# Kernel optimization log

Measured on AMD Instinct MI355X. Metric: run time of the kernel, lower is better.

## Reference

```python
import jax, jax.numpy as jnp
import numpy as np

TOP_K = 4

def setup_inputs() -> dict:
    key = jax.random.key(0)
    ks = jax.random.split(key, 10)
    s = 0.02
    return {
        "x": jax.random.normal(ks[0], (4, 1024, 2048), jnp.float32),
        "expert_bias": jnp.zeros((64,), jnp.float32),
        "router_w": jax.random.normal(ks[1], (64, 2048), jnp.float32) * s,
        "gate_w": jax.random.normal(ks[2], (8192, 2048), jnp.float32) * s,
        "up_w": jax.random.normal(ks[3], (8192, 2048), jnp.float32) * s,
        "down_w": jax.random.normal(ks[4], (2048, 8192), jnp.float32) * s,
        "w_down": jax.random.normal(ks[5], (512, 2048), jnp.float32) * s,
        "w_up": jax.random.normal(ks[6], (2048, 512), jnp.float32) * s,
        "experts_w12": jax.random.normal(ks[7], (64, 512, 2048), jnp.float32) * s,
        "experts_w3": jax.random.normal(ks[8], (64, 1024, 512), jnp.float32) * s,
    }


def reference(x, expert_bias, router_w, gate_w, up_w, down_w, w_down, w_up, experts_w12, experts_w3):
    B, S, D = x.shape
    E = router_w.shape[0]
    K = TOP_K
    h = x.reshape(-1, D)            # [N, D]
    N = h.shape[0]
    NK = N * K

    # --- router (fp32) ---
    logits = h @ router_w.T          # [N, E]
    scores = jax.nn.sigmoid(logits)
    z_loss = jnp.mean(logits * logits) * 1e-4
    sel = scores + expert_bias
    _, topk_idx = jax.lax.top_k(sel, K)                      # [N, K]
    topk_logits = jnp.take_along_axis(logits, topk_idx, axis=1)
    gating = jax.nn.softmax(topk_logits, axis=-1)            # [N, K]

    # --- shared SwiGLU expert ---
    shared = (jax.nn.silu(h @ gate_w.T) * (h @ up_w.T)) @ down_w.T   # [N, D]

    # --- bottleneck down projection ---
    hd = h @ w_down.T                # [N, bottle]
    Bn = hd.shape[1]

    # --- dispatch: sort tokens by expert, capacity max_load per expert ---
    flat = topk_idx.reshape(-1)                      # [NK]
    perm = jnp.argsort(flat)                         # stable sort
    sorted_e = flat[perm]
    counts = jnp.bincount(flat, length=E)
    ptr = jnp.cumsum(counts) - counts                # start offset per expert
    local = jnp.arange(NK) - ptr[sorted_e]           # rank within expert
    max_load = (NK // E // 8 + 6) * 8                # static python int
    num_slots = E * max_load
    mask = local < max_load
    slots = sorted_e * max_load + local
    tok = jnp.repeat(jnp.arange(N), K)               # token id per routed slot

    # reverse_map[slot] = token index (N = dummy)
    rm = jnp.full((num_slots + 1,), N, dtype=jnp.int32)
    rm = rm.at[jnp.where(mask, slots, num_slots)].set(tok[perm].astype(jnp.int32))
    reverse_map = rm[:num_slots]

    hwd = jnp.concatenate([hd, jnp.zeros((1, Bn), hd.dtype)], axis=0)
    padding = hwd[reverse_map].reshape(E, max_load, Bn)

    # --- grouped expert GEMMs ---
    h12 = jnp.einsum('emb,ebf->emf', padding, experts_w12)   # [E, L, 2*F]
    h1, h2 = jnp.split(h12, 2, axis=-1)
    pout = jnp.einsum('emf,efb->emb', jax.nn.silu(h1) * h2, experts_w3)
    pout = pout.reshape(-1, Bn)                              # [num_slots, bottle]

    # --- combine: gather back per (token, k) slot and mix with gating ---
    powd = jnp.concatenate([pout, jnp.zeros((1, Bn), pout.dtype)], axis=0)
    gm = jnp.full((NK + 1,), num_slots, dtype=jnp.int32)
    gm = gm.at[jnp.where(mask, perm, NK)].set(jnp.where(mask, slots, num_slots).astype(jnp.int32))
    gather_map = gm[:NK]
    gathered = powd[gather_map].reshape(N, K, Bn)
    routed_b = jnp.einsum('nk,nkb->nb', gating, gathered)
    routed = routed_b @ w_up.T                               # [N, D]

    # eval mode: route_scale = 1.0, moe_scale = 0.5 (one shared expert), aux_loss = 0
    out = (shared + routed) * 0.5
    return out.reshape(B, S, D), z_loss
```

## Files before the change

### kernel.cpp

```cpp
#include <hip/hip_runtime.h>
#include <math.h>

#define NTOK 4096
#define DMODEL 2048
#define ENUM 64
#define HSH 8192
#define BND 512
#define FEXP 1024
#define MAXL 304
#define EPAD 384
#define ECH 16

typedef float f32x4 __attribute__((ext_vector_type(4)));
using bf16x8 = __attribute__((ext_vector_type(8))) __bf16;

typedef const __attribute__((address_space(1))) unsigned int cgu32;
typedef __attribute__((address_space(3))) unsigned int lu32;
#define GLOAD16(g, l) __builtin_amdgcn_global_load_lds((cgu32*)(g), (lu32*)(l), 16, 0, 0)

__device__ __forceinline__ unsigned short f2bf(float f) {
    union { float f; unsigned int u; } v; v.f = f;
    unsigned int u = v.u;
    return (unsigned short)((u + 0x7FFFu + ((u >> 16) & 1u)) >> 16);
}
__device__ __forceinline__ float bf2f(unsigned short s) {
    union { unsigned int u; float f; } v; v.u = ((unsigned int)s) << 16;
    return v.f;
}

__global__ __launch_bounds__(256) void init_kernel(float* zacc, int* slot2tok, unsigned short* hdz) {
    int i = blockIdx.x * 256 + threadIdx.x;
    if (i == 0) *zacc = 0.f;
    if (i < ENUM * MAXL) slot2tok[i] = NTOK;
    if (i < BND) hdz[i] = 0;
}

__global__ __launch_bounds__(256) void convert_kernel(
    const float* __restrict__ in, unsigned short* __restrict__ out, long long n)
{
    long long stride = (long long)gridDim.x * 256 * 8;
    for (long long i = ((long long)blockIdx.x * 256 + threadIdx.x) * 8; i < n; i += stride) {
        float4 a = *(const float4*)(in + i);
        float4 b = *(const float4*)(in + i + 4);
        union { unsigned short s[8]; uint4 v; } o;
        o.s[0] = f2bf(a.x); o.s[1] = f2bf(a.y); o.s[2] = f2bf(a.z); o.s[3] = f2bf(a.w);
        o.s[4] = f2bf(b.x); o.s[5] = f2bf(b.y); o.s[6] = f2bf(b.z); o.s[7] = f2bf(b.w);
        *(uint4*)(out + i) = o.v;
    }
}

__global__ __launch_bounds__(256) void tconv_kernel(
    const float* __restrict__ in, unsigned short* __restrict__ out, int Kd, int Nd)
{
    __shared__ float t[32][33];
    size_t zoff = (size_t)blockIdx.z * Kd * Nd;
    in += zoff; out += zoff;
    int n0 = blockIdx.x * 32, k0 = blockIdx.y * 32;
    int r = threadIdx.x >> 3, c = (threadIdx.x & 7) * 4;
    float4 v = *(const float4*)(in + (size_t)(k0 + r) * Nd + n0 + c);
    t[r][c] = v.x; t[r][c + 1] = v.y; t[r][c + 2] = v.z; t[r][c + 3] = v.w;
    __syncthreads();
    ushort4 o;
    o.x = f2bf(t[c + 0][r]); o.y = f2bf(t[c + 1][r]);
    o.z = f2bf(t[c + 2][r]); o.w = f2bf(t[c + 3][r]);
    *(ushort4*)(out + (size_t)(n0 + r) * Kd + k0 + c) = o;
}

__global__ __launch_bounds__(256) void router_kernel(
    const float* __restrict__ x, const float* __restrict__ rw,
    const float* __restrict__ bias, int* __restrict__ topk_idx,
    float* __restrict__ gating, float* __restrict__ zacc)
{
    int n = blockIdx.x;
    __shared__ float hrow[DMODEL];
    __shared__ float partial[ENUM][4];
    const float* hx = x + (size_t)n * DMODEL;
    for (int i = threadIdx.x; i < DMODEL; i += 256) hrow[i] = hx[i];
    __syncthreads();
    int e = threadIdx.x & 63;
    int p = threadIdx.x >> 6;
    const float4* wr4 = (const float4*)(rw + (size_t)e * DMODEL + p * 512);
    const float4* h4 = (const float4*)(hrow + p * 512);
    float s = 0.f;
    for (int i = 0; i < 128; i++) {
        float4 a = h4[i]; float4 b = wr4[i];
        s += a.x * b.x + a.y * b.y + a.z * b.z + a.w * b.w;
    }
    partial[e][p] = s;
    __syncthreads();
    if (threadIdx.x < 64) {
        float logit = partial[e][0] + partial[e][1] + partial[e][2] + partial[e][3];
        float sel = 1.f / (1.f + expf(-logit)) + bias[e];
        float zsq = logit * logit;
        for (int off = 32; off; off >>= 1) zsq += __shfl_down(zsq, off);
        if (e == 0) atomicAdd(zacc, zsq);
        float cur = sel;
        float ch_logit[4]; int ch_idx[4];
        for (int kk = 0; kk < 4; kk++) {
            float v = cur; int idx = e;
            for (int off = 1; off < 64; off <<= 1) {
                float v2 = __shfl_xor(v, off);
                int i2 = __shfl_xor(idx, off);
                if (v2 > v || (v2 == v && i2 < idx)) { v = v2; idx = i2; }
            }
            ch_idx[kk] = idx;
            ch_logit[kk] = __shfl(logit, idx);
            if (e == idx) cur = -1e30f;
        }
        if (e == 0) {
            float mx = ch_logit[0];
            for (int kk = 1; kk < 4; kk++) mx = fmaxf(mx, ch_logit[kk]);
            float se = 0.f, ex[4];
            for (int kk = 0; kk < 4; kk++) { ex[kk] = expf(ch_logit[kk] - mx); se += ex[kk]; }
            for (int kk = 0; kk < 4; kk++) {
                topk_idx[n * 4 + kk] = ch_idx[kk];
                gating[n * 4 + kk] = ex[kk] / se;
            }
        }
    }
}

__global__ __launch_bounds__(256) void rank_kernel(
    const int* __restrict__ topk_idx, int* __restrict__ slot2tok, int* __restrict__ gmap)
{
    int e = blockIdx.x;
    __shared__ int wsum[4];
    int tid = threadIdx.x;
    int lane = tid & 63, w = tid >> 6;
    int running = 0;
    for (int c = 0; c < NTOK * 4; c += 256) {
        int i = c + tid;
        int fl = topk_idx[i];
        bool m = (fl == e);
        unsigned long long bal = __ballot(m);
        int prefix = __popcll(bal & ((1ULL << lane) - 1ULL));
        if (lane == 0) wsum[w] = __popcll(bal);
        __syncthreads();
        int wbase = 0;
        for (int j = 0; j < w; j++) wbase += wsum[j];
        int total = wsum[0] + wsum[1] + wsum[2] + wsum[3];
        if (m) {
            int rank = running + wbase + prefix;
            int tok = i >> 2;
            if (rank < MAXL) {
                slot2tok[e * MAXL + rank] = tok;
                gmap[i] = e * MAXL + rank;
            } else gmap[i] = -1;
        }
        running += total;
        __syncthreads();
    }
}

template<int GATHER, int EPI>
__global__ __launch_bounds__(256) void gemm2(
    const unsigned short* __restrict__ A, long long aZ, int lda,
    const int* __restrict__ gtab,
    const unsigned short* __restrict__ Bm, long long bZ, int ldb,
    void* __restrict__ Cb, long long cZ, int ldc,
    int M, int K)
{
    __shared__ unsigned short As[2][128 * 64];
    __shared__ unsigned short Bs[2][128 * 64];
    const int z = blockIdx.z;
    const int m0 = blockIdx.y * 128;
    const int n0 = blockIdx.x * 128;
    const int tid = threadIdx.x;
    const int lane = tid & 63;
    const int w = tid >> 6;
    const int wm = (w >> 1) * 64;
    const int wn = (w & 1) * 64;

    const unsigned short* Ab = A + (GATHER ? (size_t)0 : (size_t)z * aZ);
    const unsigned short* Bb = Bm + (size_t)z * bZ;

    size_t asrc[4], bsrc[4];
    int ldso[4];
#pragma unroll
    for (int i = 0; i < 4; i++) {
        int u = i * 256 + tid;
        int r = u >> 3;
        int ce = ((u & 7) ^ (r & 7)) * 8;
        ldso[i] = u * 8;
        if constexpr (GATHER) {
            int mr = m0 + r;
            int tok = (mr < M) ? gtab[(size_t)z * MAXL + mr] : NTOK;
            asrc[i] = (size_t)tok * lda + ce;
        } else {
            asrc[i] = (size_t)(m0 + r) * lda + ce;
        }
        bsrc[i] = (size_t)(n0 + r) * ldb + ce;
    }

    const int lrow = lane & 15;
    const int kg = lane >> 4;
    const int mk = (lrow & 7) << 4;
    int arx[4], brx[4];
#pragma unroll
    for (int t = 0; t < 4; t++) {
        arx[t] = (wm + t * 16 + lrow) * 128;
        brx[t] = (wn + t * 16 + lrow) * 128;
    }

    f32x4 acc[4][4];
#pragma unroll
    for (int a = 0; a < 4; a++)
#pragma unroll
        for (int b = 0; b < 4; b++) acc[a][b] = (f32x4)0.f;

#pragma unroll
    for (int i = 0; i < 4; i++) GLOAD16(Ab + asrc[i], &As[0][ldso[i]]);
#pragma unroll
    for (int i = 0; i < 4; i++) GLOAD16(Bb + bsrc[i], &Bs[0][ldso[i]]);
    __syncthreads();

    int cur = 0;
    for (int k0 = 0; k0 < K; k0 += 64) {
        const int kn = k0 + 64;
        if (kn < K) {
            const int nxt = cur ^ 1;
#pragma unroll
            for (int i = 0; i < 4; i++) GLOAD16(Ab + asrc[i] + kn, &As[nxt][ldso[i]]);
#pragma unroll
            for (int i = 0; i < 4; i++) GLOAD16(Bb + bsrc[i] + kn, &Bs[nxt][ldso[i]]);
        }
        const char* Abase = (const char*)&As[cur][0];
        const char* Bbase = (const char*)&Bs[cur][0];
#pragma unroll
        for (int ks = 0; ks < 2; ks++) {
            const int cb = (ks * 64 + kg * 16) ^ mk;
            bf16x8 a[4], b[4];
#pragma unroll
            for (int t = 0; t < 4; t++) {
                a[t] = *(const bf16x8*)(Abase + arx[t] + cb);
                b[t] = *(const bf16x8*)(Bbase + brx[t] + cb);
            }
#pragma unroll
            for (int ni = 0; ni < 4; ni++)
#pragma unroll
                for (int mi = 0; mi < 4; mi++)
                    acc[mi][ni] = __builtin_amdgcn_mfma_f32_16x16x32_bf16(a[mi], b[ni], acc[mi][ni], 0, 0, 0);
        }
        __syncthreads();
        cur ^= 1;
    }

    const int rb0 = m0 + wm + (kg << 2);
#pragma unroll
    for (int mi = 0; mi < 4; mi++)
#pragma unroll
        for (int ni = 0; ni < 4; ni++) {
            int col = n0 + wn + ni * 16 + lrow;
#pragma unroll
            for (int r = 0; r < 4; r++) {
                int row = rb0 + mi * 16 + r;
                if (row < M) {
                    size_t ci = (size_t)z * cZ + (size_t)row * ldc + col;
                    float v = acc[mi][ni][r];
                    if constexpr (EPI == 0) {
                        ((unsigned short*)Cb)[ci] = f2bf(v);
                    } else if constexpr (EPI == 1) {
                        unsigned short* cp = (unsigned short*)Cb + ci;
                        float g = bf2f(*cp);
                        *cp = f2bf(g / (1.f + expf(-g)) * v);
                    } else if constexpr (EPI == 2) {
                        ((float*)Cb)[ci] = v;
                    } else {
                        float* cp = (float*)Cb + ci;
                        *cp = (*cp + v) * 0.5f;
                    }
                }
            }
        }
}

__global__ __launch_bounds__(256) void siluact_kernel(
    const unsigned short* __restrict__ h12, unsigned short* __restrict__ act)
{
    int e = blockIdx.y, m = blockIdx.x;
    const unsigned short* hr = h12 + ((size_t)e * EPAD + m) * 2048;
    unsigned short* ar = act + ((size_t)e * EPAD + m) * 1024;
    int j = threadIdx.x * 4;
    ushort4 h1 = *(const ushort4*)(hr + j);
    ushort4 h2 = *(const ushort4*)(hr + 1024 + j);
    ushort4 o;
    float v;
    v = bf2f(h1.x); o.x = f2bf(v / (1.f + expf(-v)) * bf2f(h2.x));
    v = bf2f(h1.y); o.y = f2bf(v / (1.f + expf(-v)) * bf2f(h2.y));
    v = bf2f(h1.z); o.z = f2bf(v / (1.f + expf(-v)) * bf2f(h2.z));
    v = bf2f(h1.w); o.w = f2bf(v / (1.f + expf(-v)) * bf2f(h2.w));
    *(ushort4*)(ar + j) = o;
}

__global__ __launch_bounds__(256) void gather_kernel(
    const unsigned short* __restrict__ pout, const int* __restrict__ gmap,
    const float* __restrict__ gating, unsigned short* __restrict__ routed_b)
{
    int n = blockIdx.x;
    int j = threadIdx.x * 2;
    float a0 = 0.f, a1 = 0.f;
#pragma unroll
    for (int kk = 0; kk < 4; kk++) {
        int slot = gmap[n * 4 + kk];
        float g = gating[n * 4 + kk];
        if (slot >= 0) {
            const unsigned short* pr = pout + (size_t)slot * BND + j;
            a0 += g * bf2f(pr[0]);
            a1 += g * bf2f(pr[1]);
        }
    }
    routed_b[(size_t)n * BND + j] = f2bf(a0);
    routed_b[(size_t)n * BND + j + 1] = f2bf(a1);
}

__global__ void zloss_kernel(const float* zacc, float* out) {
    out[0] = zacc[0] * (1.0e-4f / (float)(NTOK * ENUM));
}

extern "C" void kernel_launch(void* const* d_in, const int* in_sizes, int n_in,
                              void* d_out, int out_size, void* d_ws, size_t ws_size,
                              hipStream_t stream)
{
    const float* x      = (const float*)d_in[0];
    const float* ebias  = (const float*)d_in[1];
    const float* rw     = (const float*)d_in[2];
    const float* gate_w = (const float*)d_in[3];
    const float* up_w   = (const float*)d_in[4];
    const float* down_w = (const float*)d_in[5];
    const float* w_down = (const float*)d_in[6];
    const float* w_up   = (const float*)d_in[7];
    const float* w12    = (const float*)d_in[8];
    const float* w3     = (const float*)d_in[9];
    float* out = (float*)d_out;

    char* ws = (char*)d_ws;
    size_t off = 0;
    auto alloc = [&](size_t b) { size_t o = off; off += (b + 255) & ~(size_t)255; return o; };
    float* zacc     = (float*)(ws + alloc(4));
    int*   topk     = (int*)(ws + alloc((size_t)NTOK * 4 * 4));
    float* gating   = (float*)(ws + alloc((size_t)NTOK * 4 * 4));
    int*   gmap     = (int*)(ws + alloc((size_t)NTOK * 4 * 4));
    int*   slot2tok = (int*)(ws + alloc((size_t)ENUM * MAXL * 4));
    unsigned short* xb     = (unsigned short*)(ws + alloc((size_t)NTOK * DMODEL * 2));
    unsigned short* hd     = (unsigned short*)(ws + alloc((size_t)(NTOK + 1) * BND * 2));
    unsigned short* rb     = (unsigned short*)(ws + alloc((size_t)NTOK * BND * 2));
    unsigned short* wdownb = (unsigned short*)(ws + alloc((size_t)BND * DMODEL * 2));
    unsigned short* wupb   = (unsigned short*)(ws + alloc((size_t)DMODEL * BND * 2));
    unsigned short* wbuf   = (unsigned short*)(ws + alloc((size_t)HSH * DMODEL * 2));
    unsigned short* H1     = (unsigned short*)(ws + alloc((size_t)NTOK * HSH * 2));
    unsigned short* h12  = H1;
    unsigned short* act  = H1 + (size_t)ECH * EPAD * 2048;
    unsigned short* pout = H1 + (size_t)ECH * EPAD * 2048 + (size_t)ECH * EPAD * 1024;

    init_kernel<<<(ENUM * MAXL + 255) / 256, 256, 0, stream>>>(zacc, slot2tok, hd + (size_t)NTOK * BND);
    router_kernel<<<NTOK, 256, 0, stream>>>(x, rw, ebias, topk, gating, zacc);
    rank_kernel<<<ENUM, 256, 0, stream>>>(topk, slot2tok, gmap);

    convert_kernel<<<1024, 256, 0, stream>>>(x, xb, (long long)NTOK * DMODEL);
    convert_kernel<<<256, 256, 0, stream>>>(w_down, wdownb, (long long)BND * DMODEL);
    convert_kernel<<<256, 256, 0, stream>>>(w_up, wupb, (long long)DMODEL * BND);

    gemm2<0, 0><<<dim3(BND / 128, NTOK / 128, 1), 256, 0, stream>>>(
        xb, 0, DMODEL, nullptr, wdownb, 0, DMODEL, hd, 0, BND, NTOK, DMODEL);

    convert_kernel<<<1024, 256, 0, stream>>>(gate_w, wbuf, (long long)HSH * DMODEL);
    gemm2<0, 0><<<dim3(HSH / 128, NTOK / 128, 1), 256, 0, stream>>>(
        xb, 0, DMODEL, nullptr, wbuf, 0, DMODEL, H1, 0, HSH, NTOK, DMODEL);
    convert_kernel<<<1024, 256, 0, stream>>>(up_w, wbuf, (long long)HSH * DMODEL);
    gemm2<0, 1><<<dim3(HSH / 128, NTOK / 128, 1), 256, 0, stream>>>(
        xb, 0, DMODEL, nullptr, wbuf, 0, DMODEL, H1, 0, HSH, NTOK, DMODEL);
    convert_kernel<<<1024, 256, 0, stream>>>(down_w, wbuf, (long long)DMODEL * HSH);
    gemm2<0, 2><<<dim3(DMODEL / 128, NTOK / 128, 1), 256, 0, stream>>>(
        H1, 0, HSH, nullptr, wbuf, 0, HSH, out, 0, DMODEL, NTOK, HSH);

    for (int c = 0; c < ENUM / ECH; c++) {
        tconv_kernel<<<dim3(2048 / 32, 512 / 32, ECH), 256, 0, stream>>>(
            w12 + (size_t)c * ECH * 512 * 2048, wbuf, 512, 2048);
        gemm2<1, 0><<<dim3(2048 / 128, 3, ECH), 256, 0, stream>>>(
            hd, 0, BND, slot2tok + (size_t)c * ECH * MAXL,
            wbuf, (long long)2048 * 512, 512,
            h12, (long long)EPAD * 2048, 2048, MAXL, BND);
        tconv_kernel<<<dim3(512 / 32, 1024 / 32, ECH), 256, 0, stream>>>(
            w3 + (size_t)c * ECH * 1024 * 512, wbuf, 1024, 512);
        siluact_kernel<<<dim3(EPAD, ECH), 256, 0, stream>>>(h12, act);
        gemm2<0, 0><<<dim3(BND / 128, 3, ECH), 256, 0, stream>>>(
            act, (long long)EPAD * FEXP, FEXP, nullptr,
            wbuf, (long long)BND * FEXP, FEXP,
            pout + (size_t)c * ECH * MAXL * BND, (long long)MAXL * BND, BND, MAXL, FEXP);
    }

    gather_kernel<<<NTOK, 256, 0, stream>>>(pout, gmap, gating, rb);

    gemm2<0, 3><<<dim3(DMODEL / 128, NTOK / 128, 1), 256, 0, stream>>>(
        rb, 0, BND, nullptr, wupb, 0, BND, out, 0, DMODEL, NTOK, BND);

    zloss_kernel<<<1, 1, 0, stream>>>(zacc, out + (size_t)NTOK * DMODEL);
}
```

Before: 1.282 ms.

## Compute router logits with split-bf16 MFMA GEMM instead of scalar fp32 dot products

Replaces the per-token scalar fp32 router kernel with a three-term split-bf16 MFMA GEMM (hi*hi + hi*lo + lo*hi) that writes partial logits, followed by a separate top-k kernel that sums them. The x hi/lo conversion is fused with the existing bf16 conversion of x. This is meant to remove the slow CUDA-core router pass over all tokens. In exchange it adds extra kernels and scratch traffic, and logits are only approximately fp32-accurate, which could flip top-k selections on near ties.

```diff
diff --git a/kernel.cpp b/kernel.cpp
--- a/kernel.cpp
+++ b/kernel.cpp
@@ -47,6 +47,47 @@
         o.s[4] = f2bf(b.x); o.s[5] = f2bf(b.y); o.s[6] = f2bf(b.z); o.s[7] = f2bf(b.w);
         *(uint4*)(out + i) = o.v;
     }
+}
+
+__global__ __launch_bounds__(256) void convert_x_kernel(
+    const float* __restrict__ in, unsigned short* __restrict__ hi,
+    unsigned short* __restrict__ lo, long long n)
+{
+    long long stride = (long long)gridDim.x * 256 * 8;
+    for (long long i = ((long long)blockIdx.x * 256 + threadIdx.x) * 8; i < n; i += stride) {
+        float4 a = *(const float4*)(in + i);
+        float4 b = *(const float4*)(in + i + 4);
+        union { unsigned short s[8]; uint4 v; } oh, ol;
+        float f[8] = {a.x, a.y, a.z, a.w, b.x, b.y, b.z, b.w};
+#pragma unroll
+        for (int j = 0; j < 8; j++) {
+            unsigned short h = f2bf(f[j]);
+            oh.s[j] = h;
+            ol.s[j] = f2bf(f[j] - bf2f(h));
+        }
+        *(uint4*)(hi + i) = oh.v;
+        *(uint4*)(lo + i) = ol.v;
+    }
+}
+
+__global__ __launch_bounds__(256) void convert_rw_kernel(
+    const float* __restrict__ rw, unsigned short* __restrict__ whi,
+    unsigned short* __restrict__ wlo)
+{
+    int i = (blockIdx.x * 256 + threadIdx.x) * 4;
+    if (i >= 128 * 2048) return;
+    ushort4 oh = {0, 0, 0, 0}, ol = {0, 0, 0, 0};
+    if (i < 64 * 2048) {
+        float4 f = *(const float4*)(rw + i);
+        float v[4] = {f.x, f.y, f.z, f.w};
+        unsigned short h;
+        h = f2bf(v[0]); oh.x = h; ol.x = f2bf(v[0] - bf2f(h));
+        h = f2bf(v[1]); oh.y = h; ol.y = f2bf(v[1] - bf2f(h));
+        h = f2bf(v[2]); oh.z = h; ol.z = f2bf(v[2] - bf2f(h));
+        h = f2bf(v[3]); oh.w = h; ol.w = f2bf(v[3] - bf2f(h));
+    }
+    *(ushort4*)(whi + i) = oh;
+    *(ushort4*)(wlo + i) = ol;
 }
 
 __global__ __launch_bounds__(256) void tconv_kernel(
@@ -66,56 +107,139 @@
     *(ushort4*)(out + (size_t)(n0 + r) * Kd + k0 + c) = o;
 }
 
-__global__ __launch_bounds__(256) void router_kernel(
-    const float* __restrict__ x, const float* __restrict__ rw,
-    const float* __restrict__ bias, int* __restrict__ topk_idx,
-    float* __restrict__ gating, float* __restrict__ zacc)
-{
-    int n = blockIdx.x;
-    __shared__ float hrow[DMODEL];
-    __shared__ float partial[ENUM][4];
-    const float* hx = x + (size_t)n * DMODEL;
-    for (int i = threadIdx.x; i < DMODEL; i += 256) hrow[i] = hx[i];
+__global__ __launch_bounds__(256) void rgemm_kernel(
+    const unsigned short* __restrict__ xb, const unsigned short* __restrict__ xlo,
+    const unsigned short* __restrict__ whi, const unsigned short* __restrict__ wlo,
+    float* __restrict__ logits)
+{
+    __shared__ unsigned short As[2][128 * 64];
+    __shared__ unsigned short Bs[2][128 * 64];
+    const int z = blockIdx.z;
+    const int m0 = blockIdx.y * 128;
+    const int tid = threadIdx.x;
+    const int lane = tid & 63;
+    const int w = tid >> 6;
+    const int wm = (w >> 1) * 64;
+    const int wn = (w & 1) * 64;
+
+    const unsigned short* Ab = (z == 2) ? xlo : xb;
+    const unsigned short* Bb = (z == 1) ? wlo : whi;
+    float* Cb = logits + (size_t)z * NTOK * 128;
+
+    size_t asrc[4], bsrc[4];
+    int ldso[4];
+#pragma unroll
+    for (int i = 0; i < 4; i++) {
+        int u = i * 256 + tid;
+        int r = u >> 3;
+        int ce = ((u & 7) ^ (r & 7)) * 8;
+        ldso[i] = u * 8;
+        asrc[i] = (size_t)(m0 + r) * DMODEL + ce;
+        bsrc[i] = (size_t)r * DMODEL + ce;
+    }
+
+    const int lrow = lane & 15;
+    const int kg = lane >> 4;
+    const int mk = (lrow & 7) << 4;
+    int arx[4], brx[4];
+#pragma unroll
+    for (int t = 0; t < 4; t++) {
+        arx[t] = (wm + t * 16 + lrow) * 128;
+        brx[t] = (wn + t * 16 + lrow) * 128;
+    }
+
+    f32x4 acc[4][4];
+#pragma unroll
+    for (int a = 0; a < 4; a++)
+#pragma unroll
+        for (int b = 0; b < 4; b++) acc[a][b] = (f32x4)0.f;
+
+#pragma unroll
+    for (int i = 0; i < 4; i++) GLOAD16(Ab + asrc[i], &As[0][ldso[i]]);
+#pragma unroll
+    for (int i = 0; i < 4; i++) GLOAD16(Bb + bsrc[i], &Bs[0][ldso[i]]);
     __syncthreads();
-    int e = threadIdx.x & 63;
-    int p = threadIdx.x >> 6;
-    const float4* wr4 = (const float4*)(rw + (size_t)e * DMODEL + p * 512);
-    const float4* h4 = (const float4*)(hrow + p * 512);
-    float s = 0.f;
-    for (int i = 0; i < 128; i++) {
-        float4 a = h4[i]; float4 b = wr4[i];
-        s += a.x * b.x + a.y * b.y + a.z * b.z + a.w * b.w;
-    }
-    partial[e][p] = s;
+
+    int cur = 0;
+    for (int k0 = 0; k0 < DMODEL; k0 += 64) {
+        const int kn = k0 + 64;
+        if (kn < DMODEL) {
+            const int nxt = cur ^ 1;
+#pragma unroll
+            for (int i = 0; i < 4; i++) GLOAD16(Ab + asrc[i] + kn, &As[nxt][ldso[i]]);
+#pragma unroll
+            for (int i = 0; i < 4; i++) GLOAD16(Bb + bsrc[i] + kn, &Bs[nxt][ldso[i]]);
+        }
+        const char* Abase = (const char*)&As[cur][0];
+        const char* Bbase = (const char*)&Bs[cur][0];
+#pragma unroll
+        for (int ks = 0; ks < 2; ks++) {
+            const int cb = (ks * 64 + kg * 16) ^ mk;
+            bf16x8 a[4], b[4];
+#pragma unroll
+            for (int t = 0; t < 4; t++) {
+                a[t] = *(const bf16x8*)(Abase + arx[t] + cb);
+                b[t] = *(const bf16x8*)(Bbase + brx[t] + cb);
+            }
+#pragma unroll
+            for (int ni = 0; ni < 4; ni++)
+#pragma unroll
+                for (int mi = 0; mi < 4; mi++)
+                    acc[mi][ni] = __builtin_amdgcn_mfma_f32_16x16x32_bf16(a[mi], b[ni], acc[mi][ni], 0, 0, 0);
+        }
+        __syncthreads();
+        cur ^= 1;
+    }
+
+    const int rb0 = m0 + wm + (kg << 2);
+#pragma unroll
+    for (int mi = 0; mi < 4; mi++)
+#pragma unroll
+        for (int ni = 0; ni < 4; ni++) {
+            int col = wn + ni * 16 + lrow;
+#pragma unroll
+            for (int r = 0; r < 4; r++)
+                Cb[(size_t)(rb0 + mi * 16 + r) * 128 + col] = acc[mi][ni][r];
+        }
+}
+
+__global__ __launch_bounds__(256) void topk_kernel(
+    const float* __restrict__ logits, const float* __restrict__ bias,
+    int* __restrict__ topk_idx, float* __restrict__ gating, float* __restrict__ zacc)
+{
+    __shared__ float zpart[4];
+    const size_t Z = (size_t)NTOK * 128;
+    int wv = threadIdx.x >> 6, lane = threadIdx.x & 63;
+    int n = blockIdx.x * 4 + wv;
+    const float* lp = logits + (size_t)n * 128 + lane;
+    float logit = lp[0] + lp[Z] + lp[2 * Z];
+    float sel = 1.f / (1.f + expf(-logit)) + bias[lane];
+    float zsq = logit * logit;
+    for (int off = 32; off; off >>= 1) zsq += __shfl_down(zsq, off);
+    if (lane == 0) zpart[wv] = zsq;
     __syncthreads();
-    if (threadIdx.x < 64) {
-        float logit = partial[e][0] + partial[e][1] + partial[e][2] + partial[e][3];
-        float sel = 1.f / (1.f + expf(-logit)) + bias[e];
-        float zsq = logit * logit;
-        for (int off = 32; off; off >>= 1) zsq += __shfl_down(zsq, off);
-        if (e == 0) atomicAdd(zacc, zsq);
-        float cur = sel;
-        float ch_logit[4]; int ch_idx[4];
+    if (threadIdx.x == 0) atomicAdd(zacc, zpart[0] + zpart[1] + zpart[2] + zpart[3]);
+    float cur = sel;
+    float ch_logit[4]; int ch_idx[4];
+    for (int kk = 0; kk < 4; kk++) {
+        float v = cur; int idx = lane;
+        for (int off = 1; off < 64; off <<= 1) {
+            float v2 = __shfl_xor(v, off);
+            int i2 = __shfl_xor(idx, off);
+            if (v2 > v || (v2 == v && i2 < idx)) { v = v2; idx = i2; }
+        }
+        ch_idx[kk] = idx;
+        ch_logit[kk] = __shfl(logit, idx);
+        if (lane == idx) cur = -1e30f;
+    }
+    if (lane == 0) {
+        float mx = ch_logit[0];
+        for (int kk = 1; kk < 4; kk++) mx = fmaxf(mx, ch_logit[kk]);
+        float se = 0.f, ex[4];
+        for (int kk = 0; kk < 4; kk++) { ex[kk] = expf(ch_logit[kk] - mx); se += ex[kk]; }
         for (int kk = 0; kk < 4; kk++) {
-            float v = cur; int idx = e;
-            for (int off = 1; off < 64; off <<= 1) {
-                float v2 = __shfl_xor(v, off);
-                int i2 = __shfl_xor(idx, off);
-                if (v2 > v || (v2 == v && i2 < idx)) { v = v2; idx = i2; }
-            }
-            ch_idx[kk] = idx;
-            ch_logit[kk] = __shfl(logit, idx);
-            if (e == idx) cur = -1e30f;
-        }
-        if (e == 0) {
-            float mx = ch_logit[0];
-            for (int kk = 1; kk < 4; kk++) mx = fmaxf(mx, ch_logit[kk]);
-            float se = 0.f, ex[4];
-            for (int kk = 0; kk < 4; kk++) { ex[kk] = expf(ch_logit[kk] - mx); se += ex[kk]; }
-            for (int kk = 0; kk < 4; kk++) {
-                topk_idx[n * 4 + kk] = ch_idx[kk];
-                gating[n * 4 + kk] = ex[kk] / se;
-            }
+            topk_idx[n * 4 + kk] = ch_idx[kk];
+            gating[n * 4 + kk] = ex[kk] / se;
         }
     }
 }
@@ -351,12 +475,19 @@
     unsigned short* h12  = H1;
     unsigned short* act  = H1 + (size_t)ECH * EPAD * 2048;
     unsigned short* pout = H1 + (size_t)ECH * EPAD * 2048 + (size_t)ECH * EPAD * 1024;
+    unsigned short* xlo    = H1;
+    float*          logits = (float*)((char*)H1 + (size_t)NTOK * DMODEL * 2);
+    unsigned short* whi    = (unsigned short*)((char*)logits + (size_t)3 * NTOK * 128 * 4);
+    unsigned short* wlo    = whi + (size_t)128 * DMODEL;
 
     init_kernel<<<(ENUM * MAXL + 255) / 256, 256, 0, stream>>>(zacc, slot2tok, hd + (size_t)NTOK * BND);
-    router_kernel<<<NTOK, 256, 0, stream>>>(x, rw, ebias, topk, gating, zacc);
+
+    convert_x_kernel<<<1024, 256, 0, stream>>>(x, xb, xlo, (long long)NTOK * DMODEL);
+    convert_rw_kernel<<<(128 * 2048 / 4 + 255) / 256, 256, 0, stream>>>(rw, whi, wlo);
+    rgemm_kernel<<<dim3(1, NTOK / 128, 3), 256, 0, stream>>>(xb, xlo, whi, wlo, logits);
+    topk_kernel<<<NTOK / 4, 256, 0, stream>>>(logits, ebias, topk, gating, zacc);
     rank_kernel<<<ENUM, 256, 0, stream>>>(topk, slot2tok, gmap);
 
-    convert_kernel<<<1024, 256, 0, stream>>>(x, xb, (long long)NTOK * DMODEL);
     convert_kernel<<<256, 256, 0, stream>>>(w_down, wdownb, (long long)BND * DMODEL);
     convert_kernel<<<256, 256, 0, stream>>>(w_up, wupb, (long long)DMODEL * BND);
 
```

Result: faster. 1.112 ms (-13.2%).
